# Kernel tuning notes

Hardware: AMD Instinct MI355X
Metric: run time of the kernel (lower is better)

The kernel has to match this reference:

```python
import jax, jax.numpy as jnp
import numpy as np

P = 100_000      # distinct products
T = 300_000      # total product nodes after repeat_interleave (sum of cnt)
NQ = 100_000     # query nodes
B = 8192         # number of sessions (segments)
QIN = 128; PIN = 128; D = 128; MSL = 50; DL = D - MSL


def setup_inputs() -> dict:
    key = jax.random.key(0)
    ks = jax.random.split(key, 12)
    # irregular repeat counts in {1..5}, tiled so sum == 3*P == T exactly (static shape)
    cnt = jnp.asarray(np.tile(np.array([1, 2, 3, 4, 5], np.int32), P // 5))
    s = 0.05
    return {
        "query_feat": jax.random.normal(ks[0], (NQ, QIN), jnp.float32),
        "product_feat": jax.random.normal(ks[1], (P, PIN), jnp.float32),
        "Wq": jax.random.normal(ks[2], (DL, QIN), jnp.float32) * s,
        "bq": jnp.zeros((DL,), jnp.float32),
        "Wp": jax.random.normal(ks[3], (DL, PIN), jnp.float32) * s,
        "bp": jnp.zeros((DL,), jnp.float32),
        "pos_table": jax.random.normal(ks[4], (MSL, MSL), jnp.float32) * s,
        "Wn": jax.random.normal(ks[5], (D, D), jnp.float32) * s,
        "bn": jnp.zeros((D,), jnp.float32),
        "Wc": jax.random.normal(ks[6], (D, D), jnp.float32) * s,
        "Wa": jax.random.normal(ks[7], (1, D), jnp.float32) * s,
        "query_pos_id": jax.random.randint(ks[8], (NQ,), 0, MSL, jnp.int32),
        "product_pos_id": jax.random.randint(ks[9], (T,), 0, MSL, jnp.int32),
        "query_batch": jax.random.randint(ks[10], (NQ,), 0, B, jnp.int32),
        "product_batch": jax.random.randint(ks[11], (P,), 0, B, jnp.int32),
        "cnt": cnt,
        "num_segments": B,
        "total_product_nodes": T,
    }


def _segment_mean(x, seg, num_segments):
    sums = jax.ops.segment_sum(x, seg, num_segments=num_segments)
    counts = jax.ops.segment_sum(jnp.ones((x.shape[0],), x.dtype), seg, num_segments=num_segments)
    return sums / jnp.maximum(counts, 1.0)[:, None]


def reference(query_feat, product_feat, Wq, bq, Wp, bp, pos_table, Wn, bn, Wc, Wa,
              query_pos_id, product_pos_id, query_batch, product_batch, cnt,
              num_segments, total_product_nodes):
    # query branch: linear -> concat positional embedding -> tanh  [NQ, D]
    qe = jnp.tanh(jnp.concatenate([query_feat @ Wq.T + bq, pos_table[query_pos_id]], axis=1))
    # product branch: linear, repeat_interleave by cnt, concat pos emb, tanh  [T, D]
    pe = product_feat @ Wp.T + bp
    pe = jnp.repeat(pe, cnt, axis=0, total_repeat_length=total_product_nodes)
    pe = jnp.tanh(jnp.concatenate([pe, pos_table[product_pos_id]], axis=1))
    pbatch = jnp.repeat(product_batch, cnt, axis=0, total_repeat_length=total_product_nodes)
    # stack nodes (products first, then queries — matches torch.concat order)
    node_emb = jnp.concatenate([pe, qe], axis=0)            # [N, D]
    node_batch = jnp.concatenate([pbatch, query_batch], axis=0)
    # coarse session representation: segment mean, broadcast back to nodes
    coarse = _segment_mean(node_emb, node_batch, num_segments)  # [B, D]
    coarse_g = coarse[node_batch]                                # [N, D]
    # attention gating
    att = jax.nn.sigmoid(node_emb @ Wn.T + bn + coarse_g @ Wc.T) @ Wa.T  # [N, 1]
    weighted = node_emb * att
    return _segment_mean(weighted, node_batch, num_segments)    # [B, D]
```

## Files before the change

kernel.cpp:

```cpp
#include <hip/hip_runtime.h>
#include <hip/hip_bf16.h>
#include <math.h>


constexpr int D   = 128;
constexpr int DL  = 78;
constexpr int MSL = 50;
constexpr int RP  = 80;

typedef __attribute__((ext_vector_type(8))) short bfrag8;
typedef __attribute__((ext_vector_type(4))) float facc4;
typedef __attribute__((ext_vector_type(4))) short short4v;

__device__ __forceinline__ float sigmoidf_(float x) {
    return 1.f / (1.f + __expf(-x));
}
__device__ __forceinline__ float ftanh(float x) {
    float e = __expf(2.f * x);
    return 1.f - 2.f * __builtin_amdgcn_rcpf(e + 1.f);
}

__device__ __forceinline__ char* ldsAddr(__hip_bfloat16* base, int row, int byte_in_row) {
    return reinterpret_cast<char*>(base) + row * 256 + (byte_in_row ^ ((row & 7) << 4));
}
__device__ __forceinline__ bfrag8 ldsR16(const __hip_bfloat16* base, int row, int byte_in_row) {
    return *reinterpret_cast<const bfrag8*>(
        reinterpret_cast<const char*>(base) + row * 256 + (byte_in_row ^ ((row & 7) << 4)));
}
__device__ __forceinline__ short4v ldsR8(const __hip_bfloat16* base, int row, int byte_in_row) {
    return *reinterpret_cast<const short4v*>(
        reinterpret_cast<const char*>(base) + row * 256 + (byte_in_row ^ ((row & 7) << 4)));
}

__device__ __forceinline__ bfrag8 cvt8(float4 a, float4 b) {
    __hip_bfloat16 t[8] = {__float2bfloat16(a.x), __float2bfloat16(a.y),
                           __float2bfloat16(a.z), __float2bfloat16(a.w),
                           __float2bfloat16(b.x), __float2bfloat16(b.y),
                           __float2bfloat16(b.z), __float2bfloat16(b.w)};
    return *reinterpret_cast<bfrag8*>(t);
}

__global__ __launch_bounds__(256) void k_tables2(
    const float* __restrict__ pos_table, const float* __restrict__ Wn,
    float* __restrict__ tpos, float* __restrict__ posWn) {
    __shared__ float tposL[MSL * MSL];
    int t = threadIdx.x;
    for (int o = t; o < MSL * MSL; o += 256) tposL[o] = tanhf(pos_table[o]);
    __syncthreads();
    if (blockIdx.x == 0)
        for (int o = t; o < MSL * MSL; o += 256) tpos[o] = tposL[o];
    for (int o = blockIdx.x * 256 + t; o < MSL * D; o += gridDim.x * 256) {
        int r = o >> 7, d = o & 127;
        float acc = 0.f;
        #pragma unroll 10
        for (int j = 0; j < MSL; ++j) acc += tposL[r * MSL + j] * Wn[d * D + DL + j];
        posWn[o] = acc;
    }
}

__global__ __launch_bounds__(256) void k_convW(
    const float* __restrict__ Wq, const float* __restrict__ Wp, const float* __restrict__ Wn,
    __hip_bfloat16* __restrict__ Wqbf, __hip_bfloat16* __restrict__ Wpbf,
    __hip_bfloat16* __restrict__ Wnbf) {
    int i = blockIdx.x * 256 + threadIdx.x;
    if (i < 80 * 128) {
        int n = i >> 7;
        Wqbf[i] = __float2bfloat16((n < DL) ? Wq[i] : 0.f);
        Wpbf[i] = __float2bfloat16((n < DL) ? Wp[i] : 0.f);
    } else if (i < 80 * 128 + 128 * 128) {
        int o = i - 80 * 128;
        int j = o & 127;
        Wnbf[o] = __float2bfloat16((j < DL) ? Wn[o] : 0.f);
    }
}

__global__ void k_scanA(const int* __restrict__ cnt, int P, int* __restrict__ chunkSum) {
    __shared__ int s[256];
    int p = blockIdx.x * 256 + threadIdx.x;
    s[threadIdx.x] = (p < P) ? cnt[p] : 0;
    __syncthreads();
    for (int st = 128; st > 0; st >>= 1) {
        if (threadIdx.x < st) s[threadIdx.x] += s[threadIdx.x + st];
        __syncthreads();
    }
    if (threadIdx.x == 0) chunkSum[blockIdx.x] = s[0];
}
__global__ __launch_bounds__(1024) void k_scanB(
    const int* __restrict__ chunkSum, int nC, int* __restrict__ chunkOff) {
    __shared__ int s[1024];
    int t = threadIdx.x;
    int carry = 0;
    for (int base = 0; base < nC; base += 1024) {
        int v = (base + t < nC) ? chunkSum[base + t] : 0;
        s[t] = v;
        __syncthreads();
        for (int st = 1; st < 1024; st <<= 1) {
            int add = (t >= st) ? s[t - st] : 0;
            __syncthreads();
            s[t] += add;
            __syncthreads();
        }
        if (base + t < nC) chunkOff[base + t] = carry + s[t] - v;
        carry += s[1023];
        __syncthreads();
    }
}
__global__ void k_scanC(const int* __restrict__ cnt, int P, const int* __restrict__ chunkOff,
                        int* __restrict__ prodOff) {
    __shared__ int s[256];
    int t = threadIdx.x;
    int p = blockIdx.x * 256 + t;
    int v = (p < P) ? cnt[p] : 0;
    s[t] = v;
    __syncthreads();
    for (int st = 1; st < 256; st <<= 1) {
        int add = (t >= st) ? s[t - st] : 0;
        __syncthreads();
        s[t] += add;
        __syncthreads();
    }
    if (p < P) prodOff[p] = chunkOff[blockIdx.x] + s[t] - v;
}

__global__ __launch_bounds__(256, 4) void k_branch2(
    const float* __restrict__ qfeat, const float* __restrict__ pfeat,
    const __hip_bfloat16* __restrict__ Wqbf, const __hip_bfloat16* __restrict__ Wpbf,
    const float* __restrict__ bq, const float* __restrict__ bp,
    const __hip_bfloat16* __restrict__ Wnbf,
    const int* __restrict__ qbatch, const int* __restrict__ pbatch,
    const int* __restrict__ qpos, const int* __restrict__ ppos,
    const int* __restrict__ cnt, const int* __restrict__ prodOff,
    int NQ, int P, int qBlocks,
    __hip_bfloat16* __restrict__ tq, __hip_bfloat16* __restrict__ tp,
    __hip_bfloat16* __restrict__ qWn, __hip_bfloat16* __restrict__ pWn,
    float* __restrict__ segsum, float* __restrict__ segcnt, int* __restrict__ hist) {
    const bool isQ = (int)blockIdx.x < qBlocks;
    const int r0 = (isQ ? blockIdx.x : blockIdx.x - qBlocks) * 64;
    const float* feat = isQ ? qfeat : pfeat;
    const __hip_bfloat16* Wbf = isQ ? Wqbf : Wpbf;
    const float* bias = isQ ? bq : bp;
    const int* batch = isQ ? qbatch : pbatch;
    const int Nrows = isQ ? NQ : P;
    __hip_bfloat16* tE  = isQ ? tq : tp;
    __hip_bfloat16* eWn = isQ ? qWn : pWn;

    __shared__ __hip_bfloat16 linL[64 * 128];
    __shared__ __hip_bfloat16 eWnL[64 * 128];
    int t = threadIdx.x;
    int l = t & 63, w = t >> 6;
    int lr = l & 15, lq = l >> 4;
    int am = w * 16 + lr;

    if (t < 64) {
        bfrag8 z = {0, 0, 0, 0, 0, 0, 0, 0};
        *reinterpret_cast<bfrag8*>(ldsAddr(linL, t, 160)) = z;
        *reinterpret_cast<bfrag8*>(ldsAddr(linL, t, 176)) = z;
    }

    int gra = r0 + am;
    const float* frow = &feat[(size_t)(gra < Nrows ? gra : Nrows - 1) * 128];
    bfrag8 a[4];
    #pragma unroll
    for (int kt = 0; kt < 4; ++kt) {
        float4 u = *reinterpret_cast<const float4*>(&frow[kt * 32 + lq * 8]);
        float4 v = *reinterpret_cast<const float4*>(&frow[kt * 32 + lq * 8 + 4]);
        a[kt] = cvt8(u, v);
    }

    facc4 c1[5];
    #pragma unroll
    for (int nt = 0; nt < 5; ++nt) { facc4 z = {0.f, 0.f, 0.f, 0.f}; c1[nt] = z; }
    #pragma unroll
    for (int nt = 0; nt < 5; ++nt) {
        #pragma unroll
        for (int kt = 0; kt < 4; ++kt) {
            bfrag8 b = *reinterpret_cast<const bfrag8*>(&Wbf[(nt * 16 + lr) * 128 + kt * 32 + lq * 8]);
            c1[nt] = __builtin_amdgcn_mfma_f32_16x16x32_bf16(a[kt], b, c1[nt], 0, 0, 0);
        }
    }

    int   bj[4];
    float mult[4];
    bool  valid[4];
    #pragma unroll
    for (int j = 0; j < 4; ++j) {
        int m = w * 16 + lq * 4 + j;
        int gr = r0 + m;
        valid[j] = gr < Nrows;
        bj[j]    = valid[j] ? batch[gr] : 0;
        mult[j]  = isQ ? 1.f : (valid[j] ? (float)cnt[gr] : 0.f);
    }
    #pragma unroll
    for (int nt = 0; nt < 5; ++nt) {
        int n = nt * 16 + lr;
        float bs = (n < DL) ? bias[n] : 0.f;
        #pragma unroll
        for (int j = 0; j < 4; ++j) {
            int m = w * 16 + lq * 4 + j;
            float tv = (n < DL) ? ftanh(c1[nt][j] + bs) : 0.f;
            *reinterpret_cast<__hip_bfloat16*>(ldsAddr(linL, m, 2 * n)) = __float2bfloat16(tv);
            if (n < DL && valid[j])
                atomicAdd(&segsum[(size_t)bj[j] * D + n], mult[j] * tv);
        }
    }
    __syncthreads();

    {
        int r = t >> 2, c = t & 3;
        int gr = r0 + r;
        #pragma unroll
        for (int j = 0; j < 5; ++j) {
            short4v v = ldsR8(linL, r, c * 40 + j * 8);
            if (gr < Nrows)
                *reinterpret_cast<short4v*>(&tE[(size_t)gr * RP + c * 20 + j * 4]) = v;
        }
    }

    bfrag8 a2[3];
    #pragma unroll
    for (int kt = 0; kt < 3; ++kt) a2[kt] = ldsR16(linL, am, kt * 64 + lq * 16);
    facc4 c2[8];
    #pragma unroll
    for (int nt = 0; nt < 8; ++nt) { facc4 z = {0.f, 0.f, 0.f, 0.f}; c2[nt] = z; }
    #pragma unroll
    for (int nt = 0; nt < 8; ++nt) {
        #pragma unroll
        for (int kt = 0; kt < 3; ++kt) {
            bfrag8 b = *reinterpret_cast<const bfrag8*>(&Wnbf[(nt * 16 + lr) * 128 + kt * 32 + lq * 8]);
            c2[nt] = __builtin_amdgcn_mfma_f32_16x16x32_bf16(a2[kt], b, c2[nt], 0, 0, 0);
        }
    }
    #pragma unroll
    for (int nt = 0; nt < 8; ++nt) {
        int d2 = nt * 16 + lr;
        #pragma unroll
        for (int j = 0; j < 4; ++j) {
            int m = w * 16 + lq * 4 + j;
            *reinterpret_cast<__hip_bfloat16*>(ldsAddr(eWnL, m, 2 * d2)) =
                __float2bfloat16(c2[nt][j]);
        }
    }
    __syncthreads();
    {
        int r = t >> 2, c = t & 3;
        int gr = r0 + r;
        #pragma unroll
        for (int j = 0; j < 4; ++j) {
            bfrag8 v = ldsR16(eWnL, r, c * 64 + j * 16);
            if (gr < Nrows)
                *reinterpret_cast<bfrag8*>(&eWn[(size_t)gr * 128 + c * 32 + j * 8]) = v;
        }
    }

    if (t < 64) {
        int gr = r0 + t;
        if (gr < Nrows) {
            int b = batch[gr];
            if (isQ) {
                atomicAdd(&segcnt[b], 1.f);
                atomicAdd(&hist[b * MSL + qpos[gr]], 1);
            } else {
                int c = cnt[gr], off2 = prodOff[gr];
                atomicAdd(&segcnt[b], (float)c);
                for (int j = 0; j < c; ++j)
                    atomicAdd(&hist[b * MSL + ppos[off2 + j]], 1);
            }
        }
    }
}

__global__ void k_possum(const int* __restrict__ hist, const float* __restrict__ tpos,
                         int B, float* __restrict__ segsum) {
    int t = threadIdx.x;
    int bb = t / MSL, k = t - bb * MSL;
    if (bb >= 5) return;
    int b = blockIdx.x * 5 + bb;
    if (b >= B) return;
    float acc = 0.f;
    for (int r = 0; r < MSL; ++r) acc += (float)hist[b * MSL + r] * tpos[r * MSL + k];
    segsum[(size_t)b * D + DL + k] = acc;
}

__global__ __launch_bounds__(256) void k_coarse(
    const float* __restrict__ segsum, const float* __restrict__ segcnt,
    const float* __restrict__ Wc, const float* __restrict__ bn, int B,
    float* __restrict__ coarseWc) {
    __shared__ __hip_bfloat16 WcL[128 * 130];
    __shared__ float cL[16 * 128];
    int t = threadIdx.x;
    int b0 = blockIdx.x * 16;
    for (int o = t; o < D * D; o += 256) {
        int d = o >> 7, k = o & 127;
        WcL[d * 130 + k] = __float2bfloat16(Wc[o]);
    }
    for (int o = t; o < 16 * D; o += 256) {
        int bb = o >> 7, d = o & 127;
        int b = b0 + bb;
        cL[o] = (b < B) ? segsum[(size_t)b * D + d] / fmaxf(segcnt[b], 1.f) : 0.f;
    }
    __syncthreads();
    for (int o = t; o < 16 * D; o += 256) {
        int bb = o >> 7, d = o & 127;
        int b = b0 + bb;
        if (b >= B) continue;
        float acc = bn[d];
        const float* cr = &cL[bb * 128];
        const __hip_bfloat16* wr = &WcL[d * 130];
        #pragma unroll 8
        for (int j = 0; j < D; ++j) acc += cr[j] * __bfloat162float(wr[j]);
        coarseWc[(size_t)b * D + d] = acc;
    }
}

__global__ __launch_bounds__(256) void k_att(
    const __hip_bfloat16* __restrict__ pWn, const __hip_bfloat16* __restrict__ tp,
    const __hip_bfloat16* __restrict__ qWn, const __hip_bfloat16* __restrict__ tq,
    const float* __restrict__ coarseWc, const float* __restrict__ posWn,
    const float* __restrict__ tpos, const float* __restrict__ Wa,
    const int* __restrict__ pbatch, const int* __restrict__ qbatch,
    const int* __restrict__ prodOff, const int* __restrict__ cnt,
    const int* __restrict__ ppos, const int* __restrict__ qpos,
    int P, int NQ, int pBlocks, float* __restrict__ out) {
    int wv = threadIdx.x >> 6, l = threadIdx.x & 63;
    if ((int)blockIdx.x < pBlocks) {
        int p = blockIdx.x * 4 + wv;
        if (p >= P) return;
        int b = pbatch[p], off = prodOff[p], c = cnt[p];
        float base0 = __bfloat162float(pWn[(size_t)p * D + l])      + coarseWc[(size_t)b * D + l];
        float base1 = __bfloat162float(pWn[(size_t)p * D + 64 + l]) + coarseWc[(size_t)b * D + 64 + l];
        float wa0 = Wa[l], wa1 = Wa[64 + l];
        float part[5];
        int   posr[5];
        #pragma unroll
        for (int j = 0; j < 5; ++j) {
            bool on = j < c;
            int pos = on ? ppos[off + j] : 0;
            posr[j] = pos;
            float z0 = base0 + posWn[pos * D + l];
            float z1 = base1 + posWn[pos * D + 64 + l];
            part[j] = on ? (sigmoidf_(z0) * wa0 + sigmoidf_(z1) * wa1) : 0.f;
        }
        #pragma unroll
        for (int m = 1; m < 64; m <<= 1) {
            #pragma unroll
            for (int j = 0; j < 5; ++j) part[j] += __shfl_xor(part[j], m, 64);
        }
        float attsum = part[0] + part[1] + part[2] + part[3] + part[4];
        float posacc = 0.f;
        if (l >= 14) {
            #pragma unroll
            for (int j = 0; j < 5; ++j)
                posacc += part[j] * tpos[posr[j] * MSL + (l - 14)];
        }
        float t0 = __bfloat162float(tp[(size_t)p * RP + l]);
        atomicAdd(&out[(size_t)b * D + l], attsum * t0);
        if (l < 14) {
            float t1 = __bfloat162float(tp[(size_t)p * RP + 64 + l]);
            atomicAdd(&out[(size_t)b * D + 64 + l], attsum * t1);
        } else {
            atomicAdd(&out[(size_t)b * D + 64 + l], posacc);
        }
    } else {
        int q = (blockIdx.x - pBlocks) * 4 + wv;
        if (q >= NQ) return;
        int b = qbatch[q], pos = qpos[q];
        float z0 = __bfloat162float(qWn[(size_t)q * D + l])      + coarseWc[(size_t)b * D + l]      + posWn[pos * D + l];
        float z1 = __bfloat162float(qWn[(size_t)q * D + 64 + l]) + coarseWc[(size_t)b * D + 64 + l] + posWn[pos * D + 64 + l];
        float part = sigmoidf_(z0) * Wa[l] + sigmoidf_(z1) * Wa[64 + l];
        #pragma unroll
        for (int m = 1; m < 64; m <<= 1) part += __shfl_xor(part, m, 64);
        float e0 = __bfloat162float(tq[(size_t)q * RP + l]);
        atomicAdd(&out[(size_t)b * D + l], part * e0);
        float e1 = (l < 14) ? __bfloat162float(tq[(size_t)q * RP + 64 + l]) : tpos[pos * MSL + (l - 14)];
        atomicAdd(&out[(size_t)b * D + 64 + l], part * e1);
    }
}

__global__ void k_final(float* __restrict__ out, const float* __restrict__ segcnt, int B) {
    int i = blockIdx.x * 256 + threadIdx.x;
    if (i < B * D) out[i] = out[i] / fmaxf(segcnt[i >> 7], 1.f);
}

extern "C" void kernel_launch(void* const* d_in, const int* in_sizes, int n_in,
                              void* d_out, int out_size, void* d_ws, size_t ws_size,
                              hipStream_t stream) {
    const float* query_feat   = (const float*)d_in[0];
    const float* product_feat = (const float*)d_in[1];
    const float* Wq = (const float*)d_in[2];
    const float* bq = (const float*)d_in[3];
    const float* Wp = (const float*)d_in[4];
    const float* bp = (const float*)d_in[5];
    const float* pos_table = (const float*)d_in[6];
    const float* Wn = (const float*)d_in[7];
    const float* bn = (const float*)d_in[8];
    const float* Wc = (const float*)d_in[9];
    const float* Wa = (const float*)d_in[10];
    const int* qpos   = (const int*)d_in[11];
    const int* ppos   = (const int*)d_in[12];
    const int* qbatch = (const int*)d_in[13];
    const int* pbatch = (const int*)d_in[14];
    const int* cnt    = (const int*)d_in[15];

    int NQ = in_sizes[11];
    int P  = in_sizes[15];
    int B  = out_size / D;
    float* out = (float*)d_out;

    char* w = (char*)d_ws;
    size_t off = 0;
    auto take = [&](size_t bytes) -> char* {
        char* p = w + off;
        off = (off + bytes + 255) & ~(size_t)255;
        return p;
    };
    float* segsum = (float*)take((size_t)B * D * 4);
    float* segcnt = (float*)take((size_t)B * 4);
    int*   hist   = (int*)  take((size_t)B * MSL * 4);
    size_t zeroBytes = off;
    float* coarseWc = (float*)take((size_t)B * D * 4);
    float* tpos  = (float*)take(MSL * MSL * 4);
    float* posWn = (float*)take(MSL * D * 4);
    __hip_bfloat16* Wqbf = (__hip_bfloat16*)take(80 * 128 * 2);
    __hip_bfloat16* Wpbf = (__hip_bfloat16*)take(80 * 128 * 2);
    __hip_bfloat16* Wnbf = (__hip_bfloat16*)take(128 * 128 * 2);
    int nC = (P + 255) / 256;
    int* chunkSum = (int*)take((size_t)nC * 4);
    int* chunkOff = (int*)take((size_t)nC * 4);
    int* prodOff  = (int*)take((size_t)P * 4);
    __hip_bfloat16* tq  = (__hip_bfloat16*)take((size_t)NQ * RP * 2);
    __hip_bfloat16* tp  = (__hip_bfloat16*)take((size_t)P * RP * 2);
    __hip_bfloat16* qWn = (__hip_bfloat16*)take((size_t)NQ * D * 2);
    __hip_bfloat16* pWn = (__hip_bfloat16*)take((size_t)P * D * 2);
    (void)ws_size; (void)n_in;

    hipMemsetAsync(segsum, 0, zeroBytes, stream);
    hipMemsetAsync(out, 0, (size_t)out_size * 4, stream);

    hipLaunchKernelGGL(k_tables2, dim3(8), dim3(256), 0, stream, pos_table, Wn, tpos, posWn);
    hipLaunchKernelGGL(k_convW, dim3((80 * 128 + 128 * 128 + 255) / 256), dim3(256), 0, stream,
                       Wq, Wp, Wn, Wqbf, Wpbf, Wnbf);
    hipLaunchKernelGGL(k_scanA, dim3(nC), dim3(256), 0, stream, cnt, P, chunkSum);
    hipLaunchKernelGGL(k_scanB, dim3(1), dim3(1024), 0, stream, chunkSum, nC, chunkOff);
    hipLaunchKernelGGL(k_scanC, dim3(nC), dim3(256), 0, stream, cnt, P, chunkOff, prodOff);

    int qBlocks = (NQ + 63) / 64, pBlocksBr = (P + 63) / 64;
    hipLaunchKernelGGL(k_branch2, dim3(qBlocks + pBlocksBr), dim3(256), 0, stream,
                       query_feat, product_feat, Wqbf, Wpbf, bq, bp, Wnbf,
                       qbatch, pbatch, qpos, ppos, cnt, prodOff, NQ, P, qBlocks,
                       tq, tp, qWn, pWn, segsum, segcnt, hist);

    hipLaunchKernelGGL(k_possum, dim3((B + 4) / 5), dim3(256), 0, stream, hist, tpos, B, segsum);
    hipLaunchKernelGGL(k_coarse, dim3((B + 15) / 16), dim3(256), 0, stream,
                       segsum, segcnt, Wc, bn, B, coarseWc);

    int pBlocksAtt = (P + 3) / 4, qBlocksAtt = (NQ + 3) / 4;
    hipLaunchKernelGGL(k_att, dim3(pBlocksAtt + qBlocksAtt), dim3(256), 0, stream,
                       pWn, tp, qWn, tq, coarseWc, posWn, tpos, Wa,
                       pbatch, qbatch, prodOff, cnt, ppos, qpos, P, NQ, pBlocksAtt, out);
    hipLaunchKernelGGL(k_final, dim3((B * D + 255) / 256), dim3(256), 0, stream, out, segcnt, B);
}
```

Before: 312.6 us.

## Replace segment-sum atomics with CSR bucketing and per-segment gather reduction

Takes the per-element float atomicAdds into segsum and segcnt out of the branch kernel. Instead it builds a CSR grouping of node rows by session using a count pass, a single-block scan and an atomic ranking pass. A new per-segment kernel then gathers the stored bf16 tanh values and reduces them, and it also derives the segment counts from the position histogram. This removes heavy atomic contention, but it adds three small kernels and reads the segment sums from bf16-rounded values. It also raises the branch kernel's launch bounds to 5 blocks per CU.

Measured after the change: 337.3 us. +7.9%, slower.

```diff
diff --git a/kernel.cpp b/kernel.cpp
--- a/kernel.cpp
+++ b/kernel.cpp
@@ -122,7 +122,48 @@
     if (p < P) prodOff[p] = chunkOff[blockIdx.x] + s[t] - v;
 }
 
-__global__ __launch_bounds__(256, 4) void k_branch2(
+__global__ void k_nodecnt(const int* __restrict__ qbatch, const int* __restrict__ pbatch,
+                          int NQ, int N, int* __restrict__ nodeCnt) {
+    int r = blockIdx.x * 256 + threadIdx.x;
+    if (r >= N) return;
+    int b = (r < NQ) ? qbatch[r] : pbatch[r - NQ];
+    atomicAdd(&nodeCnt[b], 1);
+}
+__global__ __launch_bounds__(1024) void k_scanSeg(
+    const int* __restrict__ nodeCnt, int B, int* __restrict__ segOff, int* __restrict__ cursor) {
+    __shared__ int s[1024];
+    int t = threadIdx.x;
+    int carry = 0;
+    for (int base = 0; base < B; base += 1024) {
+        int v = (base + t < B) ? nodeCnt[base + t] : 0;
+        s[t] = v;
+        __syncthreads();
+        for (int st = 1; st < 1024; st <<= 1) {
+            int add = (t >= st) ? s[t - st] : 0;
+            __syncthreads();
+            s[t] += add;
+            __syncthreads();
+        }
+        if (base + t < B) {
+            int e = carry + s[t] - v;
+            segOff[base + t] = e;
+            cursor[base + t] = e;
+        }
+        carry += s[1023];
+        __syncthreads();
+    }
+    if (t == 0) segOff[B] = carry;
+}
+__global__ void k_rank(const int* __restrict__ qbatch, const int* __restrict__ pbatch,
+                       int NQ, int N, int* __restrict__ cursor, int* __restrict__ rowOf) {
+    int r = blockIdx.x * 256 + threadIdx.x;
+    if (r >= N) return;
+    int b = (r < NQ) ? qbatch[r] : pbatch[r - NQ];
+    int slot = atomicAdd(&cursor[b], 1);
+    rowOf[slot] = r;
+}
+
+__global__ __launch_bounds__(256, 5) void k_branch2(
     const float* __restrict__ qfeat, const float* __restrict__ pfeat,
     const __hip_bfloat16* __restrict__ Wqbf, const __hip_bfloat16* __restrict__ Wpbf,
     const float* __restrict__ bq, const float* __restrict__ bp,
@@ -133,7 +174,7 @@
     int NQ, int P, int qBlocks,
     __hip_bfloat16* __restrict__ tq, __hip_bfloat16* __restrict__ tp,
     __hip_bfloat16* __restrict__ qWn, __hip_bfloat16* __restrict__ pWn,
-    float* __restrict__ segsum, float* __restrict__ segcnt, int* __restrict__ hist) {
+    int* __restrict__ hist) {
     const bool isQ = (int)blockIdx.x < qBlocks;
     const int r0 = (isQ ? blockIdx.x : blockIdx.x - qBlocks) * 64;
     const float* feat = isQ ? qfeat : pfeat;
@@ -179,17 +220,6 @@
         }
     }
 
-    int   bj[4];
-    float mult[4];
-    bool  valid[4];
-    #pragma unroll
-    for (int j = 0; j < 4; ++j) {
-        int m = w * 16 + lq * 4 + j;
-        int gr = r0 + m;
-        valid[j] = gr < Nrows;
-        bj[j]    = valid[j] ? batch[gr] : 0;
-        mult[j]  = isQ ? 1.f : (valid[j] ? (float)cnt[gr] : 0.f);
-    }
     #pragma unroll
     for (int nt = 0; nt < 5; ++nt) {
         int n = nt * 16 + lr;
@@ -199,8 +229,6 @@
             int m = w * 16 + lq * 4 + j;
             float tv = (n < DL) ? ftanh(c1[nt][j] + bs) : 0.f;
             *reinterpret_cast<__hip_bfloat16*>(ldsAddr(linL, m, 2 * n)) = __float2bfloat16(tv);
-            if (n < DL && valid[j])
-                atomicAdd(&segsum[(size_t)bj[j] * D + n], mult[j] * tv);
         }
     }
     __syncthreads();
@@ -257,11 +285,9 @@
         if (gr < Nrows) {
             int b = batch[gr];
             if (isQ) {
-                atomicAdd(&segcnt[b], 1.f);
                 atomicAdd(&hist[b * MSL + qpos[gr]], 1);
             } else {
                 int c = cnt[gr], off2 = prodOff[gr];
-                atomicAdd(&segcnt[b], (float)c);
                 for (int j = 0; j < c; ++j)
                     atomicAdd(&hist[b * MSL + ppos[off2 + j]], 1);
             }
@@ -269,16 +295,41 @@
     }
 }
 
-__global__ void k_possum(const int* __restrict__ hist, const float* __restrict__ tpos,
-                         int B, float* __restrict__ segsum) {
-    int t = threadIdx.x;
-    int bb = t / MSL, k = t - bb * MSL;
-    if (bb >= 5) return;
-    int b = blockIdx.x * 5 + bb;
-    if (b >= B) return;
-    float acc = 0.f;
-    for (int r = 0; r < MSL; ++r) acc += (float)hist[b * MSL + r] * tpos[r * MSL + k];
-    segsum[(size_t)b * D + DL + k] = acc;
+__global__ __launch_bounds__(128) void k_segsum2(
+    const __hip_bfloat16* __restrict__ tq, const __hip_bfloat16* __restrict__ tp,
+    const int* __restrict__ cnt, const int* __restrict__ rowOf,
+    const int* __restrict__ segOff, const int* __restrict__ hist,
+    const float* __restrict__ tpos, int NQ,
+    float* __restrict__ segsum, float* __restrict__ segcnt) {
+    int b = blockIdx.x, t = threadIdx.x;
+    if (t < DL) {
+        int s0 = segOff[b], s1 = segOff[b + 1];
+        float acc = 0.f;
+        for (int i = s0; i < s1; ++i) {
+            int r = rowOf[i];
+            float wv, val;
+            if (r < NQ) {
+                wv = 1.f;
+                val = __bfloat162float(tq[(size_t)r * RP + t]);
+            } else {
+                int pr = r - NQ;
+                wv = (float)cnt[pr];
+                val = __bfloat162float(tp[(size_t)pr * RP + t]);
+            }
+            acc += wv * val;
+        }
+        segsum[(size_t)b * D + t] = acc;
+    } else {
+        int k = t - DL;
+        float acc = 0.f, c = 0.f;
+        for (int r = 0; r < MSL; ++r) {
+            float h = (float)hist[b * MSL + r];
+            acc += h * tpos[r * MSL + k];
+            c += h;
+        }
+        segsum[(size_t)b * D + DL + k] = acc;
+        if (k == 0) segcnt[b] = c;
+    }
 }
 
 __global__ __launch_bounds__(256) void k_coarse(
@@ -404,6 +455,7 @@
     int NQ = in_sizes[11];
     int P  = in_sizes[15];
     int B  = out_size / D;
+    int N  = NQ + P;
     float* out = (float*)d_out;
 
     char* w = (char*)d_ws;
@@ -413,10 +465,11 @@
         off = (off + bytes + 255) & ~(size_t)255;
         return p;
     };
-    float* segsum = (float*)take((size_t)B * D * 4);
-    float* segcnt = (float*)take((size_t)B * 4);
-    int*   hist   = (int*)  take((size_t)B * MSL * 4);
+    float* segsum  = (float*)take((size_t)B * D * 4);
+    int*   hist    = (int*)  take((size_t)B * MSL * 4);
+    int*   nodeCnt = (int*)  take((size_t)B * 4);
     size_t zeroBytes = off;
+    float* segcnt   = (float*)take((size_t)B * 4);
     float* coarseWc = (float*)take((size_t)B * D * 4);
     float* tpos  = (float*)take(MSL * MSL * 4);
     float* posWn = (float*)take(MSL * D * 4);
@@ -427,6 +480,9 @@
     int* chunkSum = (int*)take((size_t)nC * 4);
     int* chunkOff = (int*)take((size_t)nC * 4);
     int* prodOff  = (int*)take((size_t)P * 4);
+    int* segOffA  = (int*)take((size_t)(B + 1) * 4);
+    int* cursor   = (int*)take((size_t)B * 4);
+    int* rowOf    = (int*)take((size_t)N * 4);
     __hip_bfloat16* tq  = (__hip_bfloat16*)take((size_t)NQ * RP * 2);
     __hip_bfloat16* tp  = (__hip_bfloat16*)take((size_t)P * RP * 2);
     __hip_bfloat16* qWn = (__hip_bfloat16*)take((size_t)NQ * D * 2);
@@ -443,13 +499,20 @@
     hipLaunchKernelGGL(k_scanB, dim3(1), dim3(1024), 0, stream, chunkSum, nC, chunkOff);
     hipLaunchKernelGGL(k_scanC, dim3(nC), dim3(256), 0, stream, cnt, P, chunkOff, prodOff);
 
+    hipLaunchKernelGGL(k_nodecnt, dim3((N + 255) / 256), dim3(256), 0, stream,
+                       qbatch, pbatch, NQ, N, nodeCnt);
+    hipLaunchKernelGGL(k_scanSeg, dim3(1), dim3(1024), 0, stream, nodeCnt, B, segOffA, cursor);
+    hipLaunchKernelGGL(k_rank, dim3((N + 255) / 256), dim3(256), 0, stream,
+                       qbatch, pbatch, NQ, N, cursor, rowOf);
+
     int qBlocks = (NQ + 63) / 64, pBlocksBr = (P + 63) / 64;
     hipLaunchKernelGGL(k_branch2, dim3(qBlocks + pBlocksBr), dim3(256), 0, stream,
                        query_feat, product_feat, Wqbf, Wpbf, bq, bp, Wnbf,
                        qbatch, pbatch, qpos, ppos, cnt, prodOff, NQ, P, qBlocks,
-                       tq, tp, qWn, pWn, segsum, segcnt, hist);
-
-    hipLaunchKernelGGL(k_possum, dim3((B + 4) / 5), dim3(256), 0, stream, hist, tpos, B, segsum);
+                       tq, tp, qWn, pWn, hist);
+
+    hipLaunchKernelGGL(k_segsum2, dim3(B), dim3(128), 0, stream,
+                       tq, tp, cnt, rowOf, segOffA, hist, tpos, NQ, segsum, segcnt);
     hipLaunchKernelGGL(k_coarse, dim3((B + 15) / 16), dim3(256), 0, stream,
                        segsum, segcnt, Wc, bn, B, coarseWc);
 
```
